# Performance work log

Measured on AMD Instinct MI355X. Metric: run time of the kernel, lower is better.

## Reference

```python
import jax, jax.numpy as jnp
import numpy as np

D, H, W = 128, 128, 128
MAX_R = 2  # static; equals min(ceil(max radius_vox), 20) given scales <= 0.01 -> radius <= 1.92
N_PTS = 100000


def quaternion_to_rotation_matrix(q):
    # q: (N, 4) as (w, x, y, z)
    q = q / jnp.linalg.norm(q, axis=-1, keepdims=True)
    w, x, y, z = q[..., 0], q[..., 1], q[..., 2], q[..., 3]
    r00 = 1 - 2 * (y * y + z * z); r01 = 2 * (x * y - w * z); r02 = 2 * (x * z + w * y)
    r10 = 2 * (x * y + w * z); r11 = 1 - 2 * (x * x + z * z); r12 = 2 * (y * z - w * x)
    r20 = 2 * (x * z - w * y); r21 = 2 * (y * z + w * x); r22 = 1 - 2 * (x * x + y * y)
    return jnp.stack([r00, r01, r02, r10, r11, r12, r20, r21, r22], axis=-1).reshape(q.shape[0], 3, 3)


def setup_inputs() -> dict:
    key = jax.random.key(0)
    k1, k2, k3, k4 = jax.random.split(key, 4)
    positions = jax.random.uniform(k1, (N_PTS, 3), minval=-1.0, maxval=1.0, dtype=jnp.float32)
    scales = jax.random.uniform(k2, (N_PTS, 3), minval=0.002, maxval=0.01, dtype=jnp.float32)
    rotations = jax.random.normal(k3, (N_PTS, 4), dtype=jnp.float32)
    density = jax.random.normal(k4, (N_PTS,), dtype=jnp.float32)
    return {"positions": positions, "scales": scales, "rotations": rotations,
            "density": density, "chunk_size": 4096}


def reference(positions, scales, rotations, density, chunk_size):
    # chunk_size only affects torch memory staging, not the math (single logical chunk here)
    shape_t = jnp.array([D, H, W], dtype=jnp.float32)
    center = (positions + 1.0) * 0.5 * shape_t - 0.5            # (N,3) voxel-space centers
    Rm = quaternion_to_rotation_matrix(rotations)                # (N,3,3)
    S_inv = 1.0 / (scales + 1e-8)                                # (N,3)
    L = Rm * S_inv[:, None, :]                                   # scale columns, as in torch R * S_inv.unsqueeze(1)
    cov_inv = jnp.einsum('nij,nkj->nik', L, L)                   # L @ L^T, (N,3,3)

    k_rng = jnp.arange(-MAX_R, MAX_R + 1)
    kz, ky, kx = jnp.meshgrid(k_rng, k_rng, k_rng, indexing='ij')
    offsets = jnp.stack([kz, ky, kx], axis=-1).reshape(-1, 3).astype(jnp.float32)  # (K,3), K=(2r+1)^3

    gc = jnp.round(center)[:, None, :] + offsets[None, :, :]     # (N,K,3) global voxel coords
    gz, gy, gx = gc[..., 0], gc[..., 1], gc[..., 2]
    valid = (gz >= 0) & (gz < D) & (gy >= 0) & (gy < H) & (gx >= 0) & (gx < W)

    diff_norm = (gc - center[:, None, :]) / (shape_t * 0.5)      # (N,K,3)
    mahal = jnp.einsum('nkd,nde,nke->nk', diff_norm, cov_inv, diff_norm)  # (N,K)
    mask = valid & (mahal <= 9.0)

    vals = jnp.where(mask, jnp.exp(-0.5 * mahal), 0.0) * density[:, None]  # (N,K)
    flat_idx = (gz.astype(jnp.int32) * (H * W) + gy.astype(jnp.int32) * W + gx.astype(jnp.int32))
    flat_idx = jnp.where(mask, flat_idx, 0)                      # masked entries carry zero value

    volume = jnp.zeros(D * H * W, dtype=jnp.float32).at[flat_idx.reshape(-1)].add(vals.reshape(-1))
    return volume.reshape(D, H, W)
```

## Files before the change

kernel.cpp:

```cpp
#include <hip/hip_runtime.h>


#define VOX_D 128
#define VOX_H 128
#define VOX_W 128
#define MAX_R 2
#define KW (2 * MAX_R + 1)

__global__ __launch_bounds__(256) void voxelize_splat(
    const float* __restrict__ positions,
    const float* __restrict__ scales,
    const float* __restrict__ rotations,
    const float* __restrict__ density,
    float* __restrict__ volume,
    int n)
{
    const int tid = blockIdx.x * blockDim.x + threadIdx.x;
    if (tid >= n * KW) return;
    const int i  = tid / KW;
    const int t0 = tid - i * KW - MAX_R;

    const float p0 = positions[3 * i + 0];
    const float p1 = positions[3 * i + 1];
    const float p2 = positions[3 * i + 2];

    const float c0 = (p0 + 1.0f) * 64.0f - 0.5f;
    const float c1 = (p1 + 1.0f) * 64.0f - 0.5f;
    const float c2 = (p2 + 1.0f) * 64.0f - 0.5f;

    const int b0 = (int)rintf(c0);
    const int b1 = (int)rintf(c1);
    const int b2 = (int)rintf(c2);

    const int g0 = b0 + t0;

    float qw = rotations[4 * i + 0];
    float qx = rotations[4 * i + 1];
    float qy = rotations[4 * i + 2];
    float qz = rotations[4 * i + 3];
    const float qn = rsqrtf(qw * qw + qx * qx + qy * qy + qz * qz);
    qw *= qn; qx *= qn; qy *= qn; qz *= qn;

    const float r00 = 1.0f - 2.0f * (qy * qy + qz * qz);
    const float r01 = 2.0f * (qx * qy - qw * qz);
    const float r02 = 2.0f * (qx * qz + qw * qy);
    const float r10 = 2.0f * (qx * qy + qw * qz);
    const float r11 = 1.0f - 2.0f * (qx * qx + qz * qz);
    const float r12 = 2.0f * (qy * qz - qw * qx);
    const float r20 = 2.0f * (qx * qz - qw * qy);
    const float r21 = 2.0f * (qy * qz + qw * qx);
    const float r22 = 1.0f - 2.0f * (qx * qx + qy * qy);

    const float s0 = scales[3 * i + 0];
    const float s1 = scales[3 * i + 1];
    const float s2 = scales[3 * i + 2];

    const float HS = 3.0f * 64.0f;
    const float h0 = HS * sqrtf(r00 * r00 * s0 * s0 + r01 * r01 * s1 * s1 + r02 * r02 * s2 * s2) + 1e-2f;
    const float h1 = HS * sqrtf(r10 * r10 * s0 * s0 + r11 * r11 * s1 * s1 + r12 * r12 * s2 * s2) + 1e-2f;
    const float h2 = HS * sqrtf(r20 * r20 * s0 * s0 + r21 * r21 * s1 * s1 + r22 * r22 * s2 * s2) + 1e-2f;

    if ((float)g0 < c0 - h0 || (float)g0 > c0 + h0) return;
    if (g0 < 0 || g0 >= VOX_D) return;

    int lo1 = (int)ceilf(c1 - h1);  if (lo1 < b1 - MAX_R) lo1 = b1 - MAX_R;  if (lo1 < 0) lo1 = 0;
    int hi1 = (int)floorf(c1 + h1); if (hi1 > b1 + MAX_R) hi1 = b1 + MAX_R;  if (hi1 > VOX_H - 1) hi1 = VOX_H - 1;
    int lo2 = (int)ceilf(c2 - h2);  if (lo2 < b2 - MAX_R) lo2 = b2 - MAX_R;  if (lo2 < 0) lo2 = 0;
    int hi2 = (int)floorf(c2 + h2); if (hi2 > b2 + MAX_R) hi2 = b2 + MAX_R;  if (hi2 > VOX_W - 1) hi2 = VOX_W - 1;
    if (lo1 > hi1 || lo2 > hi2) return;

    const float si0 = 1.0f / (s0 + 1e-8f);
    const float si1 = 1.0f / (s1 + 1e-8f);
    const float si2 = 1.0f / (s2 + 1e-8f);
    const float dens = density[i];
    const float inv_half = 1.0f / 64.0f;

    const float d0 = ((float)g0 - c0) * inv_half;
    const float a0 = r00 * d0;
    const float a1 = r01 * d0;
    const float a2 = r02 * d0;

    const int plane_base = g0 * (VOX_H * VOX_W);

    for (int g1 = lo1; g1 <= hi1; ++g1) {
        const float d1 = ((float)g1 - c1) * inv_half;
        const float e0 = a0 + r10 * d1;
        const float e1 = a1 + r11 * d1;
        const float e2 = a2 + r12 * d1;
        const int row_base = plane_base + g1 * VOX_W;
        for (int g2 = lo2; g2 <= hi2; ++g2) {
            const float d2 = ((float)g2 - c2) * inv_half;
            const float m0 = si0 * (e0 + r20 * d2);
            const float m1 = si1 * (e1 + r21 * d2);
            const float m2 = si2 * (e2 + r22 * d2);
            const float mahal = m0 * m0 + m1 * m1 + m2 * m2;
            if (mahal <= 9.0f) {
                const float val = __expf(-0.5f * mahal) * dens;
                atomicAdd(&volume[row_base + g2], val);
            }
        }
    }
}

extern "C" void kernel_launch(void* const* d_in, const int* in_sizes, int n_in,
                              void* d_out, int out_size, void* d_ws, size_t ws_size,
                              hipStream_t stream) {
    const float* positions = (const float*)d_in[0];
    const float* scales    = (const float*)d_in[1];
    const float* rotations = (const float*)d_in[2];
    const float* density   = (const float*)d_in[3];
    float* volume = (float*)d_out;

    const int n = in_sizes[0] / 3;

    hipMemsetAsync(volume, 0, (size_t)out_size * sizeof(float), stream);

    const int block = 256;
    const int total = n * KW;
    const int grid = (total + block - 1) / block;
    voxelize_splat<<<grid, block, 0, stream>>>(positions, scales, rotations,
                                               density, volume, n);
}
```

Before: 98.79 us.

## Compute exact ellipsoid row/column bounds and use four threads per splat

```diff
diff --git a/kernel.cpp b/kernel.cpp
--- a/kernel.cpp
+++ b/kernel.cpp
@@ -4,8 +4,7 @@
 #define VOX_D 128
 #define VOX_H 128
 #define VOX_W 128
-#define MAX_R 2
-#define KW (2 * MAX_R + 1)
+#define TPP 4
 
 __global__ __launch_bounds__(256) void voxelize_splat(
     const float* __restrict__ positions,
@@ -16,9 +15,9 @@
     int n)
 {
     const int tid = blockIdx.x * blockDim.x + threadIdx.x;
-    if (tid >= n * KW) return;
-    const int i  = tid / KW;
-    const int t0 = tid - i * KW - MAX_R;
+    if (tid >= n * TPP) return;
+    const int i = tid >> 2;
+    const int t = tid & 3;
 
     const float p0 = positions[3 * i + 0];
     const float p1 = positions[3 * i + 1];
@@ -27,12 +26,6 @@
     const float c0 = (p0 + 1.0f) * 64.0f - 0.5f;
     const float c1 = (p1 + 1.0f) * 64.0f - 0.5f;
     const float c2 = (p2 + 1.0f) * 64.0f - 0.5f;
-
-    const int b0 = (int)rintf(c0);
-    const int b1 = (int)rintf(c1);
-    const int b2 = (int)rintf(c2);
-
-    const int g0 = b0 + t0;
 
     float qw = rotations[4 * i + 0];
     float qx = rotations[4 * i + 1];
@@ -55,35 +48,73 @@
     const float s1 = scales[3 * i + 1];
     const float s2 = scales[3 * i + 2];
 
-    const float HS = 3.0f * 64.0f;
-    const float h0 = HS * sqrtf(r00 * r00 * s0 * s0 + r01 * r01 * s1 * s1 + r02 * r02 * s2 * s2) + 1e-2f;
-    const float h1 = HS * sqrtf(r10 * r10 * s0 * s0 + r11 * r11 * s1 * s1 + r12 * r12 * s2 * s2) + 1e-2f;
-    const float h2 = HS * sqrtf(r20 * r20 * s0 * s0 + r21 * r21 * s1 * s1 + r22 * r22 * s2 * s2) + 1e-2f;
+    const float h0 = 192.0f * sqrtf(r00 * r00 * s0 * s0 + r01 * r01 * s1 * s1
+                                    + r02 * r02 * s2 * s2) + 1e-2f;
 
-    if ((float)g0 < c0 - h0 || (float)g0 > c0 + h0) return;
-    if (g0 < 0 || g0 >= VOX_D) return;
-
-    int lo1 = (int)ceilf(c1 - h1);  if (lo1 < b1 - MAX_R) lo1 = b1 - MAX_R;  if (lo1 < 0) lo1 = 0;
-    int hi1 = (int)floorf(c1 + h1); if (hi1 > b1 + MAX_R) hi1 = b1 + MAX_R;  if (hi1 > VOX_H - 1) hi1 = VOX_H - 1;
-    int lo2 = (int)ceilf(c2 - h2);  if (lo2 < b2 - MAX_R) lo2 = b2 - MAX_R;  if (lo2 < 0) lo2 = 0;
-    int hi2 = (int)floorf(c2 + h2); if (hi2 > b2 + MAX_R) hi2 = b2 + MAX_R;  if (hi2 > VOX_W - 1) hi2 = VOX_W - 1;
-    if (lo1 > hi1 || lo2 > hi2) return;
+    int zlo = (int)ceilf(c0 - h0);
+    if (zlo < 0) zlo = 0;
+    const int g0 = zlo + t;
+    if ((float)g0 > c0 + h0 || g0 >= VOX_D) return;
 
     const float si0 = 1.0f / (s0 + 1e-8f);
     const float si1 = 1.0f / (s1 + 1e-8f);
     const float si2 = 1.0f / (s2 + 1e-8f);
-    const float dens = density[i];
-    const float inv_half = 1.0f / 64.0f;
+    const float inv_half = 0.015625f;
 
     const float d0 = ((float)g0 - c0) * inv_half;
+
     const float a0 = r00 * d0;
     const float a1 = r01 * d0;
     const float a2 = r02 * d0;
 
+    const float w0 = si0 * si0, w1 = si1 * si1, w2 = si2 * si2;
+    const float A   = w0 * r20 * r20 + w1 * r21 * r21 + w2 * r22 * r22;
+    const float b0c = w0 * r20 * a0  + w1 * r21 * a1  + w2 * r22 * a2;
+    const float b1c = w0 * r20 * r10 + w1 * r21 * r11 + w2 * r22 * r12;
+    const float cyy = w0 * r10 * r10 + w1 * r11 * r11 + w2 * r12 * r12;
+    const float cy1 = w0 * r10 * a0  + w1 * r11 * a1  + w2 * r12 * a2;
+    const float c00 = w0 * a0 * a0   + w1 * a1 * a1   + w2 * a2 * a2;
+
+    const float invA = 1.0f / A;
+
+    const float S2 = cyy - b1c * b1c * invA;
+    const float S1 = cy1 - b0c * b1c * invA;
+    const float S0 = c00 - b0c * b0c * invA - 9.001f;
+
+    float d1lo, d1hi;
+    if (S2 > 0.0f) {
+        const float discy = S1 * S1 - S2 * S0;
+        if (!(discy > 0.0f)) return;
+        const float sq = sqrtf(discy);
+        const float invS2 = 1.0f / S2;
+        d1lo = (-S1 - sq) * invS2;
+        d1hi = (-S1 + sq) * invS2;
+    } else {
+        d1lo = -0.0325f; d1hi = 0.0325f;
+    }
+
+    const float EPS = 0.125f;
+    int lo1 = (int)ceilf (c1 + 64.0f * d1lo - EPS); if (lo1 < 0) lo1 = 0;
+    int hi1 = (int)floorf(c1 + 64.0f * d1hi + EPS); if (hi1 > VOX_H - 1) hi1 = VOX_H - 1;
+    if (lo1 > hi1) return;
+
+    const float dens = density[i];
     const int plane_base = g0 * (VOX_H * VOX_W);
 
     for (int g1 = lo1; g1 <= hi1; ++g1) {
         const float d1 = ((float)g1 - c1) * inv_half;
+
+        const float Bh = b0c + b1c * d1;
+        const float Cq = c00 + (2.0f * cy1 + cyy * d1) * d1 - 9.001f;
+        const float discx = Bh * Bh - A * Cq;
+        if (!(discx > 0.0f)) continue;
+        const float sqx = sqrtf(discx);
+        const float d2lo = (-Bh - sqx) * invA;
+        const float d2hi = (-Bh + sqx) * invA;
+        int lo2 = (int)ceilf (c2 + 64.0f * d2lo - EPS); if (lo2 < 0) lo2 = 0;
+        int hi2 = (int)floorf(c2 + 64.0f * d2hi + EPS); if (hi2 > VOX_W - 1) hi2 = VOX_W - 1;
+        if (lo2 > hi2) continue;
+
         const float e0 = a0 + r10 * d1;
         const float e1 = a1 + r11 * d1;
         const float e2 = a2 + r12 * d1;
@@ -116,7 +147,7 @@
     hipMemsetAsync(volume, 0, (size_t)out_size * sizeof(float), stream);
 
     const int block = 256;
-    const int total = n * KW;
+    const int total = n * TPP;
     const int grid = (total + block - 1) / block;
     voxelize_splat<<<grid, block, 0, stream>>>(positions, scales, rotations,
                                                density, volume, n);
```

Measured after the change: 99.15 us. Within noise of the previous version (+0.4%).
